# Kernel tuning notes

Hardware: AMD Instinct MI355X
Metric: run time of the kernel (lower is better)

## Reference

```python
import jax, jax.numpy as jnp
import numpy as np


def setup_inputs() -> dict:
    key = jax.random.key(0)
    ks = jax.random.split(key, 6)
    B, U, E, D, P = 8, 1024, 1024, 256, 256
    return {
        "u_enc": jax.random.normal(ks[0], (B, U, D), dtype=jnp.float32),
        "e_enc": jax.random.normal(ks[1], (B, E, D), dtype=jnp.float32),
        "pair_enc": jax.random.normal(ks[2], (B, U, E), dtype=jnp.float32),
        "ue_mask": jax.random.uniform(ks[3], (B, U, E), dtype=jnp.float32),
        "w_kernel": jax.random.normal(ks[4], (D, P), dtype=jnp.float32) / np.sqrt(D).astype(np.float32),
        "w_bias": jnp.zeros((P,), dtype=jnp.float32),
        "bpp_w": jnp.ones((), dtype=jnp.float32),
        "bpp_b": jnp.zeros((), dtype=jnp.float32),
    }


def reference(u_enc, e_enc, pair_enc, ue_mask, w_kernel, w_bias, bpp_w, bpp_b):
    # OuterProductUpdate: shared Dense projection of u and e, then outer product.
    u_p = u_enc @ w_kernel + w_bias            # [B,U,P]
    e_p = e_enc @ w_kernel + w_bias            # [B,E,P]
    op = ue_mask * jnp.einsum('bup,bep->bue', u_p, e_p)  # [B,U,E]
    # Sigmoid gate over pair features.
    mask = ue_mask * jax.nn.sigmoid(bpp_w * pair_enc + bpp_b + op)  # [B,U,E]
    # Original: (mask[...,None] * concat(u_rep, e_rep)).sum(axis=(-2,-3)).
    # Algebraically identical without the UxEx2D intermediate:
    #   concat( sum_{u,e} mask * u_enc[u],  sum_{u,e} mask * e_enc[e] )
    u_part = jnp.einsum('bue,bud->bd', mask, u_enc)  # [B,D]
    e_part = jnp.einsum('bue,bed->bd', mask, e_enc)  # [B,D]
    return jnp.concatenate([u_part, e_part], axis=-1)  # [B,2D]
```

## Files before the change

kernel.cpp:

```cpp
#include <hip/hip_runtime.h>

#define BDIM 8
#define UDIM 1024
#define EDIM 1024
#define DDIM 256
#define PDIM 256

typedef __attribute__((ext_vector_type(8))) short bf16x8;
typedef __attribute__((ext_vector_type(4))) float f32x4;

__device__ __forceinline__ short f2bf(float x) {
    unsigned u = __float_as_uint(x);
    unsigned r = (u + 0x7FFFu + ((u >> 16) & 1u)) >> 16;
    return (short)r;
}

__device__ __forceinline__ void dma16(const void* g, void* lds) {
    __builtin_amdgcn_global_load_lds(
        (const __attribute__((address_space(1))) unsigned*)g,
        (__attribute__((address_space(3))) unsigned*)lds, 16, 0, 0);
}

#define KEEP(x) asm volatile("" :: "v"(x))

__global__ __launch_bounds__(256) void prep_kernel(
    const float* __restrict__ w, ushort* __restrict__ wT,
    float* __restrict__ sums ,
    float* __restrict__ out, int out_size)
{
    int k  = threadIdx.x;
    int n0 = blockIdx.x * 4;
    f32x4 wv = *(const f32x4*)(w + (size_t)k * PDIM + n0);
    wT[(size_t)(n0 + 0) * DDIM + k] = (ushort)f2bf(wv[0]);
    wT[(size_t)(n0 + 1) * DDIM + k] = (ushort)f2bf(wv[1]);
    wT[(size_t)(n0 + 2) * DDIM + k] = (ushort)f2bf(wv[2]);
    wT[(size_t)(n0 + 3) * DDIM + k] = (ushort)f2bf(wv[3]);
    int g = blockIdx.x * 256 + k;
    sums[g] = 0.f;
    if (g < out_size) out[g] = 0.f;
}

__global__ __launch_bounds__(256) void proj_kernel(
    const float* __restrict__ u_enc, const float* __restrict__ e_enc,
    const ushort* __restrict__ wT, const float* __restrict__ bias,
    ushort* __restrict__ u_p, ushort* __restrict__ e_p)
{
    __shared__ ushort lds_b[64 * 256];

    int bid  = blockIdx.x;
    int lin  = (bid & 7) * 128 + (bid >> 3);
    int row0 = (lin >> 2) * 64;
    int col0 = (lin & 3) * 64;

    const float* A; ushort* C;
    if (row0 < BDIM * UDIM) { A = u_enc; C = u_p; }
    else                    { A = e_enc; C = e_p; row0 -= BDIM * UDIM; }

    int tid  = threadIdx.x;
    int wave = tid >> 6, lane = tid & 63;
    int m = lane & 15, quad = lane >> 4;

    {
        int rl_base = wave * 16;
        int lr = lane >> 5;
        int cb = (lane & 31) * 16;
        #pragma unroll
        for (int j = 0; j < 8; ++j) {
            int rl = rl_base + 2 * j + lr;
            const ushort* src = wT + (size_t)(col0 + rl) * DDIM + ((cb ^ ((rl & 7) << 4)) >> 1);
            dma16(src, &lds_b[(size_t)(rl_base + 2 * j) * DDIM]);
        }
    }

    const float* aptr = A + (size_t)(row0 + wave * 16 + m) * DDIM + quad * 8;
    f32x4 a[16];
    #pragma unroll
    for (int i = 0; i < 8; ++i) {
        a[2 * i]     = *(const f32x4*)(aptr + 32 * i);
        a[2 * i + 1] = *(const f32x4*)(aptr + 32 * i + 4);
    }
    #pragma unroll
    for (int i = 0; i < 16; ++i) KEEP(a[i]);

    asm volatile("s_waitcnt vmcnt(0)" ::: "memory");
    __syncthreads();

    int rowmask = (m & 7) << 4;
    f32x4 acc[4] = {};
    #pragma unroll
    for (int i = 0; i < 8; ++i) {
        bf16x8 af;
        af[0] = f2bf(a[2*i][0]);   af[1] = f2bf(a[2*i][1]);
        af[2] = f2bf(a[2*i][2]);   af[3] = f2bf(a[2*i][3]);
        af[4] = f2bf(a[2*i+1][0]); af[5] = f2bf(a[2*i+1][1]);
        af[6] = f2bf(a[2*i+1][2]); af[7] = f2bf(a[2*i+1][3]);
        #pragma unroll
        for (int nt = 0; nt < 4; ++nt) {
            int elem = (nt * 16 + m) * DDIM + (((quad * 16 + 64 * i) ^ rowmask) >> 1);
            bf16x8 bfr = *(const bf16x8*)(lds_b + elem);
            acc[nt] = __builtin_amdgcn_mfma_f32_16x16x32_bf16(af, bfr, acc[nt], 0, 0, 0);
        }
    }

    #pragma unroll
    for (int nt = 0; nt < 4; ++nt) {
        int col = col0 + nt * 16 + m;
        float bv = bias[col];
        #pragma unroll
        for (int r = 0; r < 4; ++r) {
            int row = row0 + wave * 16 + quad * 4 + r;
            C[(size_t)row * PDIM + col] = (ushort)f2bf(acc[nt][r] + bv);
        }
    }
}

__global__ __launch_bounds__(256) void fused_kernel(
    const ushort* __restrict__ u_p, const ushort* __restrict__ e_p,
    const float* __restrict__ pair_enc, const float* __restrict__ ue_mask,
    const float* __restrict__ bpp_w_p, const float* __restrict__ bpp_b_p,
    float* __restrict__ row_sums, float* __restrict__ col_sums)
{
    __shared__ ushort lds_e[64 * 256];
    __shared__ float lds_pair[64][64];
    __shared__ float lds_mask[64][64];
    __shared__ float colred[4][64];

    int bid  = blockIdx.x;
    int b    = bid & 7;
    int tile = bid >> 3;
    int iu = tile >> 4, ie = tile & 15;
    int u0 = iu * 64, e0 = ie * 64;

    int tid  = threadIdx.x;
    int wave = tid >> 6, lane = tid & 63;
    int m = lane & 15, quad = lane >> 4;

    const float* pm = pair_enc + (size_t)b * UDIM * EDIM;
    const float* mm = ue_mask  + (size_t)b * UDIM * EDIM;
    const ushort* eb = e_p + (size_t)b * EDIM * PDIM;

    {
        int rl_base = wave * 16;
        int lr = lane >> 5;
        int cb = (lane & 31) * 16;
        #pragma unroll
        for (int j = 0; j < 8; ++j) {
            int rl = rl_base + 2 * j + lr;
            const ushort* src = eb + (size_t)(e0 + rl) * PDIM + ((cb ^ ((rl & 7) << 4)) >> 1);
            dma16(src, &lds_e[(size_t)(rl_base + 2 * j) * PDIM]);
        }
    }

    {
        int lr = lane >> 4;
        int lc = (lane & 15) * 4;
        #pragma unroll
        for (int j = 0; j < 4; ++j) {
            int r0 = wave * 16 + j * 4;
            size_t goff = (size_t)(u0 + r0 + lr) * EDIM + e0 + lc;
            dma16(pm + goff, &lds_pair[r0][0]);
            dma16(mm + goff, &lds_mask[r0][0]);
        }
    }

    const ushort* Au = u_p + (size_t)b * UDIM * PDIM + (size_t)(u0 + wave * 16 + m) * PDIM + quad * 8;
    bf16x8 af[8];
    #pragma unroll
    for (int i = 0; i < 8; ++i) af[i] = *(const bf16x8*)(Au + 32 * i);
    #pragma unroll
    for (int i = 0; i < 8; ++i) KEEP(af[i]);

    float bw = bpp_w_p[0], bb = bpp_b_p[0];

    asm volatile("s_waitcnt vmcnt(0)" ::: "memory");
    __syncthreads();

    int rowmask = (m & 7) << 4;
    f32x4 acc[4] = {};
    #pragma unroll
    for (int i = 0; i < 8; ++i) {
        #pragma unroll
        for (int nt = 0; nt < 4; ++nt) {
            int elem = (nt * 16 + m) * PDIM + (((quad * 16 + 64 * i) ^ rowmask) >> 1);
            bf16x8 bfr = *(const bf16x8*)(lds_e + elem);
            acc[nt] = __builtin_amdgcn_mfma_f32_16x16x32_bf16(af[i], bfr, acc[nt], 0, 0, 0);
        }
    }

    float rsum[4] = {0.f, 0.f, 0.f, 0.f};
    float csum[4] = {0.f, 0.f, 0.f, 0.f};
    #pragma unroll
    for (int r = 0; r < 4; ++r) {
        int row = wave * 16 + quad * 4 + r;
        #pragma unroll
        for (int nt = 0; nt < 4; ++nt) {
            int col = nt * 16 + m;
            float mv = lds_mask[row][col];
            float pv = lds_pair[row][col];
            float arg = bw * pv + bb + mv * acc[nt][r];
            float s = mv / (1.f + __expf(-arg));
            rsum[r]  += s;
            csum[nt] += s;
        }
    }

    #pragma unroll
    for (int r = 0; r < 4; ++r) {
        float v = rsum[r];
        v += __shfl_xor(v, 1); v += __shfl_xor(v, 2);
        v += __shfl_xor(v, 4); v += __shfl_xor(v, 8);
        if (m == 0)
            atomicAdd(&row_sums[(size_t)b * UDIM + u0 + wave * 16 + quad * 4 + r], v);
    }

    #pragma unroll
    for (int nt = 0; nt < 4; ++nt) {
        float v = csum[nt];
        v += __shfl_xor(v, 16); v += __shfl_xor(v, 32);
        if (quad == 0) colred[wave][nt * 16 + m] = v;
    }
    __syncthreads();

    if (tid < 64) {
        float v = colred[0][tid] + colred[1][tid] + colred[2][tid] + colred[3][tid];
        atomicAdd(&col_sums[(size_t)b * EDIM + e0 + tid], v);
    }
}

__global__ __launch_bounds__(256) void finish_kernel(
    const float* __restrict__ u_enc, const float* __restrict__ e_enc,
    const float* __restrict__ row_sums, const float* __restrict__ col_sums,
    float* __restrict__ out)
{
    int b = blockIdx.x;
    int half = blockIdx.y;
    int chunk = blockIdx.z;
    int d = threadIdx.x;

    const float* enc = half ? e_enc : u_enc;
    const float* s   = half ? col_sums : row_sums;

    int base = chunk * 32;
    float ev[32];
    #pragma unroll
    for (int j = 0; j < 32; ++j)
        ev[j] = enc[(size_t)(b * UDIM + base + j) * DDIM + d];
    #pragma unroll
    for (int j = 0; j < 32; ++j) KEEP(ev[j]);

    float acc = 0.f;
    #pragma unroll
    for (int j = 0; j < 32; ++j)
        acc += s[(size_t)b * UDIM + base + j] * ev[j];

    atomicAdd(&out[(size_t)b * 2 * DDIM + half * DDIM + d], acc);
}

extern "C" void kernel_launch(void* const* d_in, const int* in_sizes, int n_in,
                              void* d_out, int out_size, void* d_ws, size_t ws_size,
                              hipStream_t stream)
{
    const float* u_enc    = (const float*)d_in[0];
    const float* e_enc    = (const float*)d_in[1];
    const float* pair_enc = (const float*)d_in[2];
    const float* ue_mask  = (const float*)d_in[3];
    const float* w_kernel = (const float*)d_in[4];
    const float* w_bias   = (const float*)d_in[5];
    const float* bpp_w    = (const float*)d_in[6];
    const float* bpp_b    = (const float*)d_in[7];
    float* out = (float*)d_out;

    ushort* u_p = (ushort*)d_ws;
    ushort* e_p = u_p + (size_t)BDIM * UDIM * PDIM;
    ushort* wT  = e_p + (size_t)BDIM * EDIM * PDIM;
    float* row_sums = (float*)(wT + (size_t)DDIM * PDIM);
    float* col_sums = row_sums + BDIM * UDIM;

    prep_kernel<<<dim3(64), 256, 0, stream>>>(w_kernel, wT, row_sums, out, out_size);

    proj_kernel<<<dim3(1024), 256, 0, stream>>>(u_enc, e_enc, wT, w_bias, u_p, e_p);

    fused_kernel<<<dim3(2048), 256, 0, stream>>>(u_p, e_p, pair_enc, ue_mask,
                                                 bpp_w, bpp_b, row_sums, col_sums);

    finish_kernel<<<dim3(BDIM, 2, 32), 256, 0, stream>>>(u_enc, e_enc, row_sums, col_sums, out);
}
```

Before: 152.4 us.

## Process four E-tiles per block with double-buffered LDS prefetch

Each fused-kernel block now handles a 64-row U tile across four consecutive 64-column E tiles instead of one. The next tile's e_p, pair and mask data are loaded into a second LDS buffer while the current tile is computed. This reuses the U fragments held in registers and cuts row-sum atomics fourfold. It also shrinks the grid from 2048 to 512 blocks and doubles LDS use, which may lower occupancy and latency hiding. Extra barriers are added inside each iteration.

```diff
diff --git a/kernel.cpp b/kernel.cpp
--- a/kernel.cpp
+++ b/kernel.cpp
@@ -120,16 +120,18 @@
     const float* __restrict__ bpp_w_p, const float* __restrict__ bpp_b_p,
     float* __restrict__ row_sums, float* __restrict__ col_sums)
 {
-    __shared__ ushort lds_e[64 * 256];
-    __shared__ float lds_pair[64][64];
-    __shared__ float lds_mask[64][64];
+    __shared__ ushort lds_e[2][64 * 256];
+    __shared__ float lds_pair[2][64][64];
+    __shared__ float lds_mask[2][64][64];
     __shared__ float colred[4][64];
 
     int bid  = blockIdx.x;
     int b    = bid & 7;
     int tile = bid >> 3;
-    int iu = tile >> 4, ie = tile & 15;
-    int u0 = iu * 64, e0 = ie * 64;
+    int iu   = tile >> 2;
+    int eg   = tile & 3;
+    int u0   = iu * 64;
+    int e0g  = eg * 256;
 
     int tid  = threadIdx.x;
     int wave = tid >> 6, lane = tid & 63;
@@ -139,29 +141,29 @@
     const float* mm = ue_mask  + (size_t)b * UDIM * EDIM;
     const ushort* eb = e_p + (size_t)b * EDIM * PDIM;
 
-    {
-        int rl_base = wave * 16;
-        int lr = lane >> 5;
-        int cb = (lane & 31) * 16;
-        #pragma unroll
-        for (int j = 0; j < 8; ++j) {
-            int rl = rl_base + 2 * j + lr;
-            const ushort* src = eb + (size_t)(e0 + rl) * PDIM + ((cb ^ ((rl & 7) << 4)) >> 1);
-            dma16(src, &lds_e[(size_t)(rl_base + 2 * j) * PDIM]);
-        }
-    }
-
-    {
-        int lr = lane >> 4;
-        int lc = (lane & 15) * 4;
-        #pragma unroll
-        for (int j = 0; j < 4; ++j) {
-            int r0 = wave * 16 + j * 4;
-            size_t goff = (size_t)(u0 + r0 + lr) * EDIM + e0 + lc;
-            dma16(pm + goff, &lds_pair[r0][0]);
-            dma16(mm + goff, &lds_mask[r0][0]);
-        }
-    }
+    int srl  = wave * 16 + (lane >> 5);
+    int scb  = (lane & 31) * 16;
+    int plr  = lane >> 4;
+    int plc  = (lane & 15) * 4;
+    #define STAGE_TILE(t, buf) {                                               \
+        int e0 = e0g + (t) * 64;                                               \
+        _Pragma("unroll")                                                      \
+        for (int j = 0; j < 8; ++j) {                                          \
+            int rl = srl + 2 * j;                                              \
+            const ushort* src = eb + (size_t)(e0 + rl) * PDIM                  \
+                                + ((scb ^ ((rl & 7) << 4)) >> 1);              \
+            dma16(src, &lds_e[buf][(size_t)(wave * 16 + 2 * j) * PDIM]);       \
+        }                                                                      \
+        _Pragma("unroll")                                                      \
+        for (int j = 0; j < 4; ++j) {                                          \
+            int r0 = wave * 16 + j * 4;                                        \
+            size_t goff = (size_t)(u0 + r0 + plr) * EDIM + e0 + plc;           \
+            dma16(pm + goff, &lds_pair[buf][r0][0]);                           \
+            dma16(mm + goff, &lds_mask[buf][r0][0]);                           \
+        }                                                                      \
+    }
+
+    STAGE_TILE(0, 0);
 
     const ushort* Au = u_p + (size_t)b * UDIM * PDIM + (size_t)(u0 + wave * 16 + m) * PDIM + quad * 8;
     bf16x8 af[8];
@@ -171,36 +173,60 @@
     for (int i = 0; i < 8; ++i) KEEP(af[i]);
 
     float bw = bpp_w_p[0], bb = bpp_b_p[0];
-
-    asm volatile("s_waitcnt vmcnt(0)" ::: "memory");
-    __syncthreads();
-
     int rowmask = (m & 7) << 4;
-    f32x4 acc[4] = {};
-    #pragma unroll
-    for (int i = 0; i < 8; ++i) {
+
+    float rsum[4] = {0.f, 0.f, 0.f, 0.f};
+
+    #pragma unroll
+    for (int t = 0; t < 4; ++t) {
+        int buf = t & 1;
+
+        __builtin_amdgcn_s_barrier();
+        if (t < 3) STAGE_TILE(t + 1, buf ^ 1);
+        __builtin_amdgcn_sched_barrier(0);
+        if (t < 3) asm volatile("s_waitcnt vmcnt(16)" ::: "memory");
+        else       asm volatile("s_waitcnt vmcnt(0)"  ::: "memory");
+        __builtin_amdgcn_sched_barrier(0);
+        __builtin_amdgcn_s_barrier();
+
+        f32x4 acc[4] = {};
+        #pragma unroll
+        for (int i = 0; i < 8; ++i) {
+            #pragma unroll
+            for (int nt = 0; nt < 4; ++nt) {
+                int elem = (nt * 16 + m) * PDIM + (((quad * 16 + 64 * i) ^ rowmask) >> 1);
+                bf16x8 bfr = *(const bf16x8*)(&lds_e[buf][0] + elem);
+                acc[nt] = __builtin_amdgcn_mfma_f32_16x16x32_bf16(af[i], bfr, acc[nt], 0, 0, 0);
+            }
+        }
+
+        float csum[4] = {0.f, 0.f, 0.f, 0.f};
+        #pragma unroll
+        for (int r = 0; r < 4; ++r) {
+            int row = wave * 16 + quad * 4 + r;
+            #pragma unroll
+            for (int nt = 0; nt < 4; ++nt) {
+                int col = nt * 16 + m;
+                float mv = lds_mask[buf][row][col];
+                float pv = lds_pair[buf][row][col];
+                float arg = bw * pv + bb + mv * acc[nt][r];
+                float s = mv / (1.f + __expf(-arg));
+                rsum[r]  += s;
+                csum[nt] += s;
+            }
+        }
+
         #pragma unroll
         for (int nt = 0; nt < 4; ++nt) {
-            int elem = (nt * 16 + m) * PDIM + (((quad * 16 + 64 * i) ^ rowmask) >> 1);
-            bf16x8 bfr = *(const bf16x8*)(lds_e + elem);
-            acc[nt] = __builtin_amdgcn_mfma_f32_16x16x32_bf16(af[i], bfr, acc[nt], 0, 0, 0);
-        }
-    }
-
-    float rsum[4] = {0.f, 0.f, 0.f, 0.f};
-    float csum[4] = {0.f, 0.f, 0.f, 0.f};
-    #pragma unroll
-    for (int r = 0; r < 4; ++r) {
-        int row = wave * 16 + quad * 4 + r;
-        #pragma unroll
-        for (int nt = 0; nt < 4; ++nt) {
-            int col = nt * 16 + m;
-            float mv = lds_mask[row][col];
-            float pv = lds_pair[row][col];
-            float arg = bw * pv + bb + mv * acc[nt][r];
-            float s = mv / (1.f + __expf(-arg));
-            rsum[r]  += s;
-            csum[nt] += s;
+            float v = csum[nt];
+            v += __shfl_xor(v, 16); v += __shfl_xor(v, 32);
+            if (quad == 0) colred[wave][nt * 16 + m] = v;
+        }
+        asm volatile("s_waitcnt lgkmcnt(0)" ::: "memory");
+        __builtin_amdgcn_s_barrier();
+        if (tid < 64) {
+            float v = colred[0][tid] + colred[1][tid] + colred[2][tid] + colred[3][tid];
+            atomicAdd(&col_sums[(size_t)b * EDIM + e0g + t * 64 + tid], v);
         }
     }
 
@@ -212,19 +238,7 @@
         if (m == 0)
             atomicAdd(&row_sums[(size_t)b * UDIM + u0 + wave * 16 + quad * 4 + r], v);
     }
-
-    #pragma unroll
-    for (int nt = 0; nt < 4; ++nt) {
-        float v = csum[nt];
-        v += __shfl_xor(v, 16); v += __shfl_xor(v, 32);
-        if (quad == 0) colred[wave][nt * 16 + m] = v;
-    }
-    __syncthreads();
-
-    if (tid < 64) {
-        float v = colred[0][tid] + colred[1][tid] + colred[2][tid] + colred[3][tid];
-        atomicAdd(&col_sums[(size_t)b * EDIM + e0 + tid], v);
-    }
+    #undef STAGE_TILE
 }
 
 __global__ __launch_bounds__(256) void finish_kernel(
@@ -280,8 +294,8 @@
 
     proj_kernel<<<dim3(1024), 256, 0, stream>>>(u_enc, e_enc, wT, w_bias, u_p, e_p);
 
-    fused_kernel<<<dim3(2048), 256, 0, stream>>>(u_p, e_p, pair_enc, ue_mask,
-                                                 bpp_w, bpp_b, row_sums, col_sums);
+    fused_kernel<<<dim3(512), 256, 0, stream>>>(u_p, e_p, pair_enc, ue_mask,
+                                                bpp_w, bpp_b, row_sums, col_sums);
 
     finish_kernel<<<dim3(BDIM, 2, 32), 256, 0, stream>>>(u_enc, e_enc, row_sums, col_sums, out);
 }
```

After: 154.4 us. No clear change (+1.4%).

## Replace row/col sum atomics with per-tile partial buffers and pack projection stores

Applied to the files above, without the earlier changes.

The fused kernel now writes per-tile row and column partial sums to dedicated slices instead of issuing atomicAdds. The finish kernel then reduces the 16 partials per position into shared memory before its weighted sum. This removes atomic contention and the zero-init of the sum buffers, at the cost of more workspace and extra reads in finish. Separately, the projection epilogue packs four bf16 outputs into one 8-byte store. That permutes the P columns identically for u_p and e_p, which the contraction over P tolerates.

```diff
diff --git a/kernel.cpp b/kernel.cpp
--- a/kernel.cpp
+++ b/kernel.cpp
@@ -8,6 +8,7 @@
 
 typedef __attribute__((ext_vector_type(8))) short bf16x8;
 typedef __attribute__((ext_vector_type(4))) float f32x4;
+typedef __attribute__((ext_vector_type(4))) ushort u16x4;
 
 __device__ __forceinline__ short f2bf(float x) {
     unsigned u = __float_as_uint(x);
@@ -25,7 +26,6 @@
 
 __global__ __launch_bounds__(256) void prep_kernel(
     const float* __restrict__ w, ushort* __restrict__ wT,
-    float* __restrict__ sums ,
     float* __restrict__ out, int out_size)
 {
     int k  = threadIdx.x;
@@ -36,7 +36,6 @@
     wT[(size_t)(n0 + 2) * DDIM + k] = (ushort)f2bf(wv[2]);
     wT[(size_t)(n0 + 3) * DDIM + k] = (ushort)f2bf(wv[3]);
     int g = blockIdx.x * 256 + k;
-    sums[g] = 0.f;
     if (g < out_size) out[g] = 0.f;
 }
 
@@ -103,14 +102,13 @@
     }
 
     #pragma unroll
-    for (int nt = 0; nt < 4; ++nt) {
-        int col = col0 + nt * 16 + m;
-        float bv = bias[col];
-        #pragma unroll
-        for (int r = 0; r < 4; ++r) {
-            int row = row0 + wave * 16 + quad * 4 + r;
-            C[(size_t)row * PDIM + col] = (ushort)f2bf(acc[nt][r] + bv);
-        }
+    for (int r = 0; r < 4; ++r) {
+        int row = row0 + wave * 16 + quad * 4 + r;
+        u16x4 pk;
+        #pragma unroll
+        for (int nt = 0; nt < 4; ++nt)
+            pk[nt] = (ushort)f2bf(acc[nt][r] + bias[col0 + nt * 16 + m]);
+        *(u16x4*)(C + (size_t)row * PDIM + col0 + 4 * m) = pk;
     }
 }
 
@@ -118,7 +116,8 @@
     const ushort* __restrict__ u_p, const ushort* __restrict__ e_p,
     const float* __restrict__ pair_enc, const float* __restrict__ ue_mask,
     const float* __restrict__ bpp_w_p, const float* __restrict__ bpp_b_p,
-    float* __restrict__ row_sums, float* __restrict__ col_sums)
+    float* __restrict__ row_part ,
+    float* __restrict__ col_part )
 {
     __shared__ ushort lds_e[64 * 256];
     __shared__ float lds_pair[64][64];
@@ -210,7 +209,7 @@
         v += __shfl_xor(v, 1); v += __shfl_xor(v, 2);
         v += __shfl_xor(v, 4); v += __shfl_xor(v, 8);
         if (m == 0)
-            atomicAdd(&row_sums[(size_t)b * UDIM + u0 + wave * 16 + quad * 4 + r], v);
+            row_part[((size_t)b * 16 + ie) * UDIM + u0 + wave * 16 + quad * 4 + r] = v;
     }
 
     #pragma unroll
@@ -223,24 +222,34 @@
 
     if (tid < 64) {
         float v = colred[0][tid] + colred[1][tid] + colred[2][tid] + colred[3][tid];
-        atomicAdd(&col_sums[(size_t)b * EDIM + e0 + tid], v);
+        col_part[((size_t)b * 16 + iu) * EDIM + e0 + tid] = v;
     }
 }
 
 __global__ __launch_bounds__(256) void finish_kernel(
     const float* __restrict__ u_enc, const float* __restrict__ e_enc,
-    const float* __restrict__ row_sums, const float* __restrict__ col_sums,
+    const float* __restrict__ row_part, const float* __restrict__ col_part,
     float* __restrict__ out)
 {
+    __shared__ float s_lds[32];
+
     int b = blockIdx.x;
     int half = blockIdx.y;
     int chunk = blockIdx.z;
     int d = threadIdx.x;
 
-    const float* enc = half ? e_enc : u_enc;
-    const float* s   = half ? col_sums : row_sums;
+    const float* enc  = half ? e_enc   : u_enc;
+    const float* part = half ? col_part : row_part;
 
     int base = chunk * 32;
+    if (d < 32) {
+        float s = 0.f;
+        #pragma unroll
+        for (int p = 0; p < 16; ++p)
+            s += part[((size_t)b * 16 + p) * UDIM + base + d];
+        s_lds[d] = s;
+    }
+
     float ev[32];
     #pragma unroll
     for (int j = 0; j < 32; ++j)
@@ -248,10 +257,12 @@
     #pragma unroll
     for (int j = 0; j < 32; ++j) KEEP(ev[j]);
 
+    __syncthreads();
+
     float acc = 0.f;
     #pragma unroll
     for (int j = 0; j < 32; ++j)
-        acc += s[(size_t)b * UDIM + base + j] * ev[j];
+        acc += s_lds[j] * ev[j];
 
     atomicAdd(&out[(size_t)b * 2 * DDIM + half * DDIM + d], acc);
 }
@@ -273,15 +284,15 @@
     ushort* u_p = (ushort*)d_ws;
     ushort* e_p = u_p + (size_t)BDIM * UDIM * PDIM;
     ushort* wT  = e_p + (size_t)BDIM * EDIM * PDIM;
-    float* row_sums = (float*)(wT + (size_t)DDIM * PDIM);
-    float* col_sums = row_sums + BDIM * UDIM;
-
-    prep_kernel<<<dim3(64), 256, 0, stream>>>(w_kernel, wT, row_sums, out, out_size);
+    float* row_part = (float*)(wT + (size_t)DDIM * PDIM);
+    float* col_part = row_part + (size_t)BDIM * 16 * UDIM;
+
+    prep_kernel<<<dim3(64), 256, 0, stream>>>(w_kernel, wT, out, out_size);
 
     proj_kernel<<<dim3(1024), 256, 0, stream>>>(u_enc, e_enc, wT, w_bias, u_p, e_p);
 
     fused_kernel<<<dim3(2048), 256, 0, stream>>>(u_p, e_p, pair_enc, ue_mask,
-                                                 bpp_w, bpp_b, row_sums, col_sums);
-
-    finish_kernel<<<dim3(BDIM, 2, 32), 256, 0, stream>>>(u_enc, e_enc, row_sums, col_sums, out);
-}
+                                                 bpp_w, bpp_b, row_part, col_part);
+
+    finish_kernel<<<dim3(BDIM, 2, 32), 256, 0, stream>>>(u_enc, e_enc, row_part, col_part, out);
+}
```

Measured after the change: 148.6 us. 1.03x faster.
